# Kernel tuning notes

Hardware: AMD Instinct MI355X
Metric: run time of the kernel (lower is better)

Reference implementation:

```python
import jax, jax.numpy as jnp
import numpy as np

B, S, E, H, VP, L, T = 256, 256, 1024, 1024, 8, 64, 16


def setup_inputs() -> dict:
    key = jax.random.key(0)
    ks = jax.random.split(key, 10)
    image = jax.random.normal(ks[0], (B, S, E), jnp.float32)
    view_position = jax.random.uniform(ks[1], (B, VP), jnp.float32)
    label = (jax.random.uniform(ks[2], (B, T + 1, L)) > 0.5).astype(jnp.float32)
    # lengths sorted descending (length_sorted_rnn decorator), max forced to T+1
    length = jnp.sort(jax.random.randint(ks[3], (B,), 2, T + 2))[::-1]
    length = length.at[0].set(T + 1)
    def lin(k, out_d, in_d):
        return jax.random.normal(k, (out_d, in_d), jnp.float32) * (1.0 / np.sqrt(in_d)).astype(np.float32)
    IN = E + VP + 1 + L  # 1097: lstm_sizes = [embedding, view_position, 1, label]
    FC_OUT = L + H + 1 + 1  # 1090: fc_sizes = [label, hidden, 1, 1]
    return {
        'image': image, 'view_position': view_position, 'label': label, 'length': length,
        'W_h': lin(ks[4], H, E), 'b_h': jnp.zeros((H,), jnp.float32),
        'W_m': lin(ks[5], H, E), 'b_m': jnp.zeros((H,), jnp.float32),
        'W_ih': lin(ks[6], 4 * H, IN), 'W_hh': lin(ks[7], 4 * H, H),
        'b_ih': jnp.zeros((4 * H,), jnp.float32), 'b_hh': jnp.zeros((4 * H,), jnp.float32),
        'W_fc': lin(ks[8], FC_OUT, H), 'b_fc': jnp.zeros((FC_OUT,), jnp.float32),
    }


def reference(image, view_position, label, length, W_h, b_h, W_m, b_m,
              W_ih, W_hh, b_ih, b_hh, W_fc, b_fc):
    # Dropout is identity (inference). image: (B,S,E)
    image_mean = image.mean(axis=1)                      # (B,E)
    h0 = jnp.tanh(image_mean @ W_h.T + b_h)              # (B,H)
    m0 = jnp.tanh(image_mean @ W_m.T + b_m)              # (B,H)
    n_steps = label.shape[1] - 1
    bsz = image_mean.shape[0]

    def step(carry, inp):
        h, m = carry
        lab_t, t = inp
        begin = jnp.where(t == 0, 1.0, 0.0) * jnp.ones((bsz, 1), image_mean.dtype)
        x = jnp.concatenate([image_mean, view_position, begin, lab_t], axis=1)  # (B, 1097)
        gates = x @ W_ih.T + b_ih + h @ W_hh.T + b_hh    # (B, 4H)
        i, f, g, o = jnp.split(gates, 4, axis=1)
        m2 = jax.nn.sigmoid(f) * m + jax.nn.sigmoid(i) * jnp.tanh(g)
        h2 = jax.nn.sigmoid(o) * jnp.tanh(m2)
        out = h2 @ W_fc.T + b_fc                         # (B, L+H+2)
        topic = jax.nn.relu(out[:, L:L + H])
        stop = jax.nn.sigmoid(out[:, L + H:L + H + 1])
        temp = jnp.exp(out[:, L + H + 1:])
        return (h2, m2), jnp.concatenate([topic, stop, temp], axis=1)

    labels_tm = jnp.swapaxes(label[:, :n_steps], 0, 1)   # (T,B,L) time-major
    _, outs = jax.lax.scan(step, (h0, m0), (labels_tm, jnp.arange(n_steps)))
    # pad_sequence semantics: entries with t >= length-1 are zero padding
    mask = (jnp.arange(n_steps)[:, None] < (length - 1)[None, :]).astype(outs.dtype)
    return outs * mask[:, :, None]                       # (T, B, H+2) = [topic|stop|temp]
```

## Files before the change

### kernel.cpp

```cpp
#include <hip/hip_runtime.h>
#include <stdint.h>

typedef unsigned short u16;
typedef __attribute__((ext_vector_type(8))) short v8s;
typedef __attribute__((ext_vector_type(4))) float v4f;

__device__ __forceinline__ u16 f2bf(float f) {
  uint32_t x = __float_as_uint(f);
  return (u16)((x + 0x7fffu + ((x >> 16) & 1u)) >> 16);
}
__device__ __forceinline__ float bf2f(u16 u) {
  return __uint_as_float(((uint32_t)u) << 16);
}
__device__ __forceinline__ float sigf(float x) { return 1.f / (1.f + __expf(-x)); }

__device__ __forceinline__ v4f mfma16(v8s a, v8s b, v4f c) {
  return __builtin_amdgcn_mfma_f32_16x16x32_bf16(a, b, c, 0, 0, 0);
}

__device__ __forceinline__ void gll16(const u16* src, u16* ldsdst) {
  __builtin_amdgcn_global_load_lds(
      reinterpret_cast<__attribute__((address_space(1))) uint32_t*>(
          reinterpret_cast<uintptr_t>(src)),
      reinterpret_cast<__attribute__((address_space(3))) uint32_t*>(
          reinterpret_cast<uintptr_t>(ldsdst)),
      16, 0, 0);
}

__device__ __forceinline__ size_t fpoff(int row, int k, int KT) {
  return ((size_t)(((row >> 4) * KT + (k >> 6)) * 2 + ((k >> 5) & 1)) * 64 +
          ((k >> 3) & 3) * 16 + (row & 15)) * 8 + (k & 7);
}

__device__ __forceinline__ void load8(const float* p, float* f) {
  float4 a = *(const float4*)p;
  float4 b = *(const float4*)(p + 4);
  f[0]=a.x; f[1]=a.y; f[2]=a.z; f[3]=a.w; f[4]=b.x; f[5]=b.y; f[6]=b.z; f[7]=b.w;
}
__device__ __forceinline__ void store8bf(u16* dst, const float* f) {
  u16 t[8];
#pragma unroll
  for (int i = 0; i < 8; ++i) t[i] = f2bf(f[i]);
  *(v8s*)dst = *(const v8s*)t;
}

__global__ __launch_bounds__(256) void k_zero(unsigned* __restrict__ ctr) {
  ctr[blockIdx.x * 256 + threadIdx.x] = 0u;
}

__global__ __launch_bounds__(256) void k_convert_mean(
    const float* __restrict__ Wh, const float* __restrict__ Wm,
    const float* __restrict__ Wih, const float* __restrict__ Whh,
    const float* __restrict__ Wfc, const float* __restrict__ label,
    const float* __restrict__ image,
    u16* __restrict__ wcomb, u16* __restrict__ whhb, u16* __restrict__ wfcb,
    u16* __restrict__ wlabb, u16* __restrict__ labb,
    float4* __restrict__ pacc) {
  const int bid = blockIdx.x, tid = threadIdx.x;
  if (bid >= 5952) {
    int bi = bid - 5952;
    int b = bi >> 3, oct = bi & 7;
    const float4* src =
        (const float4*)image + (size_t)b * 65536 + (size_t)oct * 32 * 256 + tid;
    float4 s = make_float4(0.f, 0.f, 0.f, 0.f);
#pragma unroll 8
    for (int ss = 0; ss < 32; ++ss) {
      float4 v = src[(size_t)ss * 256];
      s.x += v.x; s.y += v.y; s.z += v.z; s.w += v.w;
    }
    pacc[(size_t)bi * 256 + tid] = s;
    return;
  }
  int64_t u = (int64_t)bid * 256 + tid;
  float f[8];
  if (u < 786432) {
    int lu = (int)u;
    int r15 = lu & 15, q = (lu >> 4) & 3, s = (lu >> 6) & 1, tile = lu >> 7;
    int tk = tile & 15, tr = tile >> 4;
    int row = tr * 16 + r15, k = tk * 64 + s * 32 + q * 8;
    if (row < 1024) load8(Wh + (size_t)row * 1024 + k, f);
    else if (row < 2048) load8(Wm + (size_t)(row - 1024) * 1024 + k, f);
    else {
      const float* p = Wih + (size_t)(row - 2048) * 1097 + k;
#pragma unroll
      for (int i = 0; i < 8; ++i) f[i] = p[i];
    }
    store8bf(wcomb + (size_t)lu * 8, f);
  } else if (u < 1310720) {
    int lu = (int)(u - 786432);
    int r15 = lu & 15, q = (lu >> 4) & 3, s = (lu >> 6) & 1, tile = lu >> 7;
    int tk = tile & 15, tr = tile >> 4;
    int row = tr * 16 + r15, k = tk * 64 + s * 32 + q * 8;
    load8(Whh + (size_t)row * 1024 + k, f);
    store8bf(whhb + (size_t)lu * 8, f);
  } else if (u < 1458176) {
    int lu = (int)(u - 1310720);
    int r15 = lu & 15, q = (lu >> 4) & 3, s = (lu >> 6) & 1, tile = lu >> 7;
    int tk = tile & 15, tr = tile >> 4;
    int row = tr * 16 + r15, k = tk * 64 + s * 32 + q * 8;
    if (row < 1090) load8(Wfc + (size_t)row * 1024 + k, f);
    else {
#pragma unroll
      for (int i = 0; i < 8; ++i) f[i] = 0.f;
    }
    store8bf(wfcb + (size_t)lu * 8, f);
  } else if (u < 1490944) {
    int lu = (int)(u - 1458176);
    int r15 = lu & 15, q = (lu >> 4) & 3, s = (lu >> 6) & 1, tile = lu >> 7;
    int row = tile * 16 + r15, k = s * 32 + q * 8;
    const float* p = Wih + (size_t)row * 1097 + 1033 + k;
#pragma unroll
    for (int i = 0; i < 8; ++i) f[i] = p[i];
    store8bf(wlabb + (size_t)lu * 8, f);
  } else {
    int lu = (int)(u - 1490944);
    int r15 = lu & 15, q = (lu >> 4) & 3, s = (lu >> 6) & 1, tile = lu >> 7;
    int row = tile * 16 + r15, k = s * 32 + q * 8;
    int t = row >> 8, b = row & 255;
    load8(label + ((size_t)b * 17 + t) * 64 + k, f);
    store8bf(labb + (size_t)lu * 8, f);
  }
}

__global__ __launch_bounds__(256) void k_mean2(const float4* __restrict__ pacc,
                                               u16* __restrict__ meanbf) {
  int b = blockIdx.x, tid = threadIdx.x;
  float4 s = make_float4(0.f, 0.f, 0.f, 0.f);
#pragma unroll
  for (int q = 0; q < 8; ++q) {
    float4 v = pacc[((size_t)b * 8 + q) * 256 + tid];
    s.x += v.x; s.y += v.y; s.z += v.z; s.w += v.w;
  }
  const float inv = 1.f / 256.f;
  int k = tid * 4;
  ushort4 o;
  o.x = f2bf(s.x * inv); o.y = f2bf(s.y * inv);
  o.z = f2bf(s.z * inv); o.w = f2bf(s.w * inv);
  *(ushort4*)&meanbf[fpoff(b, k, 16)] = o;
}

__global__ __launch_bounds__(256) void k_gemm_init(
    const u16* __restrict__ meanbf, const u16* __restrict__ wcomb,
    const float* __restrict__ bh, const float* __restrict__ bm,
    const float* __restrict__ bih, const float* __restrict__ bhh,
    const float* __restrict__ vp, const float* __restrict__ Wih,
    u16* __restrict__ hbuf, float* __restrict__ mbuf, float* __restrict__ basebuf) {
  __shared__ alignas(16) u16 lA[4 * 1024];
  __shared__ alignas(16) u16 lB[4 * 1024];
  const int tid = threadIdx.x, lane = tid & 63, wid = tid >> 6;
  const int bm0 = (blockIdx.x & 3) * 64;
  const int bn0 = (blockIdx.x >> 2) * 64;
  const int wr = wid >> 1, wc = wid & 1;
  v4f acc[2][2];
#pragma unroll
  for (int i = 0; i < 2; ++i)
#pragma unroll
    for (int j = 0; j < 2; ++j) acc[i][j] = (v4f){0.f, 0.f, 0.f, 0.f};

  for (int kt = 0; kt < 16; ++kt) {
    const u16* asrc = meanbf + ((size_t)((bm0 >> 4) + wid) * 16 + kt) * 1024 + lane * 8;
    gll16(asrc, lA + wid * 1024);
    gll16(asrc + 512, lA + wid * 1024 + 512);
    const u16* bsrc = wcomb + ((size_t)((bn0 >> 4) + wid) * 16 + kt) * 1024 + lane * 8;
    gll16(bsrc, lB + wid * 1024);
    gll16(bsrc + 512, lB + wid * 1024 + 512);
    __syncthreads();
#pragma unroll
    for (int s = 0; s < 2; ++s) {
      v8s a0 = *(const v8s*)&lA[(size_t)(wr * 2) * 1024 + s * 512 + lane * 8];
      v8s a1 = *(const v8s*)&lA[(size_t)(wr * 2 + 1) * 1024 + s * 512 + lane * 8];
      v8s b0 = *(const v8s*)&lB[(size_t)(wc * 2) * 1024 + s * 512 + lane * 8];
      v8s b1 = *(const v8s*)&lB[(size_t)(wc * 2 + 1) * 1024 + s * 512 + lane * 8];
      acc[0][0] = mfma16(a0, b0, acc[0][0]);
      acc[0][1] = mfma16(a0, b1, acc[0][1]);
      acc[1][0] = mfma16(a1, b0, acc[1][0]);
      acc[1][1] = mfma16(a1, b1, acc[1][1]);
    }
    __syncthreads();
  }
#pragma unroll
  for (int fm = 0; fm < 2; ++fm)
#pragma unroll
    for (int fn = 0; fn < 2; ++fn)
#pragma unroll
      for (int rg = 0; rg < 4; ++rg) {
        int row = bm0 + wr * 32 + fm * 16 + ((lane >> 4) << 2) + rg;
        int col = bn0 + wc * 32 + fn * 16 + (lane & 15);
        float v = acc[fm][fn][rg];
        if (col < 1024) {
          hbuf[fpoff(row, col, 16)] = f2bf(tanhf(v + bh[col]));
        } else if (col < 2048) {
          int nn = col - 1024;
          mbuf[(size_t)row * 1024 + nn] = tanhf(v + bm[nn]);
        } else {
          int j = col - 2048;
          float sv = v + bih[j] + bhh[j];
#pragma unroll
          for (int q = 0; q < 8; ++q)
            sv += vp[row * 8 + q] * Wih[(size_t)j * 1097 + 1024 + q];
          basebuf[(size_t)row * 4096 + j] = sv;
        }
      }
}

__global__ __launch_bounds__(256) void k_basefull(
    const u16* __restrict__ labb, const u16* __restrict__ wlabb,
    const float* __restrict__ basebuf, const float* __restrict__ Wih,
    u16* __restrict__ bfull) {
  __shared__ alignas(16) u16 lA[4 * 1024];
  __shared__ alignas(16) u16 lB[4 * 1024];
  const int tid = threadIdx.x, lane = tid & 63, wid = tid >> 6;
  const int bm0 = (blockIdx.x & 63) * 64;
  const int bn0 = (blockIdx.x >> 6) * 64;
  const int wr = wid >> 1, wc = wid & 1;
  v4f acc[2][2];
#pragma unroll
  for (int i = 0; i < 2; ++i)
#pragma unroll
    for (int j = 0; j < 2; ++j) acc[i][j] = (v4f){0.f, 0.f, 0.f, 0.f};

  const u16* asrc = labb + (size_t)((bm0 >> 4) + wid) * 1024 + lane * 8;
  gll16(asrc, lA + wid * 1024);
  gll16(asrc + 512, lA + wid * 1024 + 512);
  const u16* bsrc = wlabb + (size_t)((bn0 >> 4) + wid) * 1024 + lane * 8;
  gll16(bsrc, lB + wid * 1024);
  gll16(bsrc + 512, lB + wid * 1024 + 512);
  __syncthreads();
#pragma unroll
  for (int s = 0; s < 2; ++s) {
    v8s a0 = *(const v8s*)&lA[(size_t)(wr * 2) * 1024 + s * 512 + lane * 8];
    v8s a1 = *(const v8s*)&lA[(size_t)(wr * 2 + 1) * 1024 + s * 512 + lane * 8];
    v8s b0 = *(const v8s*)&lB[(size_t)(wc * 2) * 1024 + s * 512 + lane * 8];
    v8s b1 = *(const v8s*)&lB[(size_t)(wc * 2 + 1) * 1024 + s * 512 + lane * 8];
    acc[0][0] = mfma16(a0, b0, acc[0][0]);
    acc[0][1] = mfma16(a0, b1, acc[0][1]);
    acc[1][0] = mfma16(a1, b0, acc[1][0]);
    acc[1][1] = mfma16(a1, b1, acc[1][1]);
  }
#pragma unroll
  for (int fm = 0; fm < 2; ++fm)
#pragma unroll
    for (int fn = 0; fn < 2; ++fn)
#pragma unroll
      for (int rg = 0; rg < 4; ++rg) {
        int r = bm0 + wr * 32 + fm * 16 + ((lane >> 4) << 2) + rg;
        int j = bn0 + wc * 32 + fn * 16 + (lane & 15);
        int t = r >> 8, b = r & 255;
        float v = acc[fm][fn][rg] + basebuf[(size_t)b * 4096 + j];
        if (t == 0) v += Wih[(size_t)j * 1097 + 1032];
        bfull[(size_t)r * 4096 + j] = f2bf(v);
      }
}

__global__ __launch_bounds__(256, 1) void k_steps(
    const u16* __restrict__ whhb, const u16* __restrict__ bfull,
    const float* __restrict__ mbuf, u16* __restrict__ hbuf,
    unsigned* __restrict__ ctr) {
  __shared__ alignas(16) u16 lA[64 * 512];
  __shared__ alignas(16) float lact[4][32 * 33];
  const int tid = threadIdx.x, lane = tid & 63, wid = tid >> 6;
  const int blk = blockIdx.x;
  const int n0idx = (blk & 7) * 4 + (blk >> 6);
  const int n0 = n0idx * 32;
  const int grp = (blk >> 3) & 7;
  const int b0 = grp * 32;
  const int atr = b0 >> 4;

  const int tr0 = wid * 64 + (n0 >> 4);
  v8s breg[16][2][2];
#pragma unroll
  for (int kt = 0; kt < 16; ++kt)
#pragma unroll
    for (int s = 0; s < 2; ++s)
#pragma unroll
      for (int j = 0; j < 2; ++j)
        breg[kt][s][j] =
            *(const v8s*)&whhb[((size_t)(tr0 + j) * 16 + kt) * 1024 + s * 512 + lane * 8];

  const int rowm = tid >> 3;
  const int nql = (tid & 7) * 4;
  const int b = b0 + rowm;
  const int n = n0 + nql;
  float4 mreg = *(const float4*)&mbuf[(size_t)b * 1024 + n];

  for (int t = 0; t < 16; ++t) {
    if (t > 0) {
      const unsigned* f = &ctr[((t - 1) * 8 + grp) * 32];
      for (int it = 0; it < (1 << 18); ++it) {
        unsigned v = __hip_atomic_load(&f[lane & 31], __ATOMIC_RELAXED,
                                       __HIP_MEMORY_SCOPE_AGENT);
        if (__ballot(v == 0u) == 0ull) break;
        __builtin_amdgcn_s_sleep(1);
      }
    }
    const u16* hsrc = hbuf + (size_t)t * 262144;
#pragma unroll
    for (int ii = 0; ii < 16; ++ii) {
      const int c = wid * 16 + ii;
      const int i = c >> 5, kt = (c >> 1) & 15, s = c & 1;
      gll16(hsrc + ((size_t)(atr + i) * 16 + kt) * 1024 + s * 512 + lane * 8,
            lA + c * 512);
    }
    const u16* bb = bfull + (size_t)t * 1048576 + (size_t)b * 4096 + n;
    ushort4 ui = *(const ushort4*)(bb);
    ushort4 uf = *(const ushort4*)(bb + 1024);
    ushort4 ug = *(const ushort4*)(bb + 2048);
    ushort4 uo = *(const ushort4*)(bb + 3072);
    __syncthreads();

    v4f acc[2][2];
#pragma unroll
    for (int i = 0; i < 2; ++i)
#pragma unroll
      for (int j = 0; j < 2; ++j) acc[i][j] = (v4f){0.f, 0.f, 0.f, 0.f};
#pragma unroll
    for (int kt = 0; kt < 16; ++kt)
#pragma unroll
      for (int s = 0; s < 2; ++s) {
        v8s a0 = *(const v8s*)&lA[(size_t)((0 * 16 + kt) * 2 + s) * 512 + lane * 8];
        v8s a1 = *(const v8s*)&lA[(size_t)((1 * 16 + kt) * 2 + s) * 512 + lane * 8];
        acc[0][0] = mfma16(a0, breg[kt][s][0], acc[0][0]);
        acc[0][1] = mfma16(a0, breg[kt][s][1], acc[0][1]);
        acc[1][0] = mfma16(a1, breg[kt][s][0], acc[1][0]);
        acc[1][1] = mfma16(a1, breg[kt][s][1], acc[1][1]);
      }

#pragma unroll
    for (int fm = 0; fm < 2; ++fm)
#pragma unroll
      for (int fn = 0; fn < 2; ++fn)
#pragma unroll
        for (int rg = 0; rg < 4; ++rg) {
          int rr = fm * 16 + ((lane >> 4) << 2) + rg;
          int cc = fn * 16 + (lane & 15);
          lact[wid][rr * 33 + cc] = acc[fm][fn][rg];
        }
    __syncthreads();

    float m2a[4];
    u16 h2a[4];
#pragma unroll
    for (int q = 0; q < 4; ++q) {
      float gi = lact[0][rowm * 33 + nql + q] + bf2f(((const u16*)&ui)[q]);
      float gf = lact[1][rowm * 33 + nql + q] + bf2f(((const u16*)&uf)[q]);
      float gg = lact[2][rowm * 33 + nql + q] + bf2f(((const u16*)&ug)[q]);
      float go = lact[3][rowm * 33 + nql + q] + bf2f(((const u16*)&uo)[q]);
      float mov = ((const float*)&mreg)[q];
      float m2 = sigf(gf) * mov + sigf(gi) * tanhf(gg);
      float h2 = sigf(go) * tanhf(m2);
      m2a[q] = m2;
      h2a[q] = f2bf(h2);
    }
    mreg = make_float4(m2a[0], m2a[1], m2a[2], m2a[3]);
    ushort4 ho;
    ho.x = h2a[0]; ho.y = h2a[1]; ho.z = h2a[2]; ho.w = h2a[3];
    unsigned long long hv;
    __builtin_memcpy(&hv, &ho, 8);
    __hip_atomic_store(
        reinterpret_cast<unsigned long long*>(
            &hbuf[(size_t)(t + 1) * 262144 + fpoff(b, n, 16)]),
        hv, __ATOMIC_RELAXED, __HIP_MEMORY_SCOPE_AGENT);

    if (t < 15) {
      __syncthreads();
      if (tid == 0)
        __hip_atomic_store(&ctr[(t * 8 + grp) * 32 + n0idx], 1u,
                           __ATOMIC_RELAXED, __HIP_MEMORY_SCOPE_AGENT);
    }
  }
}

__global__ __launch_bounds__(256) void k_fc(
    const u16* __restrict__ hall, const u16* __restrict__ wfcb,
    const float* __restrict__ bfc, const int* __restrict__ length,
    float* __restrict__ out) {
  __shared__ alignas(16) u16 lA[4 * 1024];
  __shared__ alignas(16) u16 lB[4 * 1024];
  const int tid = threadIdx.x, lane = tid & 63, wid = tid >> 6;
  const int bm0 = (int)(blockIdx.x % 64) * 64;
  const int bn0 = (int)(blockIdx.x / 64) * 64;
  const int wr = wid >> 1, wc = wid & 1;
  v4f acc[2][2];
#pragma unroll
  for (int i = 0; i < 2; ++i)
#pragma unroll
    for (int j = 0; j < 2; ++j) acc[i][j] = (v4f){0.f, 0.f, 0.f, 0.f};

  for (int kt = 0; kt < 16; ++kt) {
    const u16* asrc = hall + ((size_t)((bm0 >> 4) + wid) * 16 + kt) * 1024 + lane * 8;
    gll16(asrc, lA + wid * 1024);
    gll16(asrc + 512, lA + wid * 1024 + 512);
    const u16* bsrc = wfcb + ((size_t)((bn0 >> 4) + wid) * 16 + kt) * 1024 + lane * 8;
    gll16(bsrc, lB + wid * 1024);
    gll16(bsrc + 512, lB + wid * 1024 + 512);
    __syncthreads();
#pragma unroll
    for (int s = 0; s < 2; ++s) {
      v8s a0 = *(const v8s*)&lA[(size_t)(wr * 2) * 1024 + s * 512 + lane * 8];
      v8s a1 = *(const v8s*)&lA[(size_t)(wr * 2 + 1) * 1024 + s * 512 + lane * 8];
      v8s b0 = *(const v8s*)&lB[(size_t)(wc * 2) * 1024 + s * 512 + lane * 8];
      v8s b1 = *(const v8s*)&lB[(size_t)(wc * 2 + 1) * 1024 + s * 512 + lane * 8];
      acc[0][0] = mfma16(a0, b0, acc[0][0]);
      acc[0][1] = mfma16(a0, b1, acc[0][1]);
      acc[1][0] = mfma16(a1, b0, acc[1][0]);
      acc[1][1] = mfma16(a1, b1, acc[1][1]);
    }
    __syncthreads();
  }
#pragma unroll
  for (int fm = 0; fm < 2; ++fm)
#pragma unroll
    for (int fn = 0; fn < 2; ++fn)
#pragma unroll
      for (int rg = 0; rg < 4; ++rg) {
        int r = bm0 + wr * 32 + fm * 16 + ((lane >> 4) << 2) + rg;
        int j = bn0 + wc * 32 + fn * 16 + (lane & 15);
        if (j < 64 || j >= 1090) continue;
        int t = r >> 8, b = r & 255;
        float v = acc[fm][fn][rg] + bfc[j];
        int c;
        if (j < 1088) { c = j - 64; v = fmaxf(v, 0.f); }
        else if (j == 1088) { c = 1024; v = 1.f / (1.f + expf(-v)); }
        else { c = 1025; v = expf(v); }
        if (t >= length[b] - 1) v = 0.f;
        out[((size_t)t * 256 + b) * 1026 + c] = v;
      }
}

extern "C" void kernel_launch(void* const* d_in, const int* in_sizes, int n_in,
                              void* d_out, int out_size, void* d_ws, size_t ws_size,
                              hipStream_t stream) {
  (void)in_sizes; (void)n_in; (void)out_size; (void)ws_size;
  const float* image  = (const float*)d_in[0];
  const float* vp     = (const float*)d_in[1];
  const float* label  = (const float*)d_in[2];
  const int*   length = (const int*)d_in[3];
  const float* Wh  = (const float*)d_in[4];
  const float* bh  = (const float*)d_in[5];
  const float* Wm  = (const float*)d_in[6];
  const float* bm  = (const float*)d_in[7];
  const float* Wih = (const float*)d_in[8];
  const float* Whh = (const float*)d_in[9];
  const float* bih = (const float*)d_in[10];
  const float* bhh = (const float*)d_in[11];
  const float* Wfc = (const float*)d_in[12];
  const float* bfc = (const float*)d_in[13];
  float* out = (float*)d_out;
  char* ws = (char*)d_ws;

  size_t off = 0;
  u16* wcomb  = (u16*)(ws + off); off += (size_t)6144 * 1024 * 2;
  u16* whhb   = (u16*)(ws + off); off += (size_t)4096 * 1024 * 2;
  u16* wfcb   = (u16*)(ws + off); off += (size_t)1152 * 1024 * 2;
  u16* wlabb  = (u16*)(ws + off); off += (size_t)4096 * 64 * 2;
  u16* labb   = (u16*)(ws + off); off += (size_t)4096 * 64 * 2;
  u16* meanbf = (u16*)(ws + off); off += (size_t)256 * 1024 * 2;
  u16* hbuf   = (u16*)(ws + off); off += (size_t)17 * 256 * 1024 * 2;
  float* mbuf    = (float*)(ws + off); off += (size_t)256 * 1024 * 4;
  float* basebuf = (float*)(ws + off); off += (size_t)256 * 4096 * 4;
  u16* bfull  = (u16*)(ws + off); off += (size_t)16 * 256 * 4096 * 2;
  unsigned* ctr = (unsigned*)(ws + off); off += 4096 * 4;
  float4* pacc = (float4*)bfull;

  k_zero<<<16, 256, 0, stream>>>(ctr);
  k_convert_mean<<<8000, 256, 0, stream>>>(Wh, Wm, Wih, Whh, Wfc, label, image,
                                           wcomb, whhb, wfcb, wlabb, labb, pacc);
  k_mean2<<<256, 256, 0, stream>>>(pacc, meanbf);
  k_gemm_init<<<384, 256, 0, stream>>>(meanbf, wcomb, bh, bm, bih, bhh, vp, Wih,
                                       hbuf, mbuf, basebuf);
  k_basefull<<<4096, 256, 0, stream>>>(labb, wlabb, basebuf, Wih, bfull);
  k_steps<<<256, 256, 0, stream>>>(whhb, bfull, mbuf, hbuf, ctr);
  k_fc<<<1152, 256, 0, stream>>>(hbuf + (size_t)256 * 1024, wfcb, bfc, length, out);
}
```

Baseline: 232.2 us.

## Split h-tile loads into two halves, stage gate bias via LDS, fold zeroing

The k_zero launch is removed and the counter zeroing is folded into extra blocks of k_convert_mean. In the recurrent step kernel, the LDS load of the hidden state is split into two K-halves with partial vmcnt waits, so MFMA work on the first half can start while the second half is still arriving. The per-step gate bias is now fetched by async global-to-LDS loads instead of per-thread register loads. The hand-written waitcnt counts and sched barriers are fragile and depend on the exact number of outstanding loads.

Result: faster. 225.6 us (-2.8%).

```diff
diff --git a/kernel.cpp b/kernel.cpp
--- a/kernel.cpp
+++ b/kernel.cpp
@@ -44,10 +44,6 @@
   *(v8s*)dst = *(const v8s*)t;
 }
 
-__global__ __launch_bounds__(256) void k_zero(unsigned* __restrict__ ctr) {
-  ctr[blockIdx.x * 256 + threadIdx.x] = 0u;
-}
-
 __global__ __launch_bounds__(256) void k_convert_mean(
     const float* __restrict__ Wh, const float* __restrict__ Wm,
     const float* __restrict__ Wih, const float* __restrict__ Whh,
@@ -55,8 +51,12 @@
     const float* __restrict__ image,
     u16* __restrict__ wcomb, u16* __restrict__ whhb, u16* __restrict__ wfcb,
     u16* __restrict__ wlabb, u16* __restrict__ labb,
-    float4* __restrict__ pacc) {
+    float4* __restrict__ pacc, unsigned* __restrict__ ctr) {
   const int bid = blockIdx.x, tid = threadIdx.x;
+  if (bid >= 8000) {
+    ctr[(bid - 8000) * 256 + tid] = 0u;
+    return;
+  }
   if (bid >= 5952) {
     int bi = bid - 5952;
     int b = bi >> 3, oct = bi & 7;
@@ -257,6 +257,7 @@
     const float* __restrict__ mbuf, u16* __restrict__ hbuf,
     unsigned* __restrict__ ctr) {
   __shared__ alignas(16) u16 lA[64 * 512];
+  __shared__ alignas(16) u16 lBias[8 * 512];
   __shared__ alignas(16) float lact[4][32 * 33];
   const int tid = threadIdx.x, lane = tid & 63, wid = tid >> 6;
   const int blk = blockIdx.x;
@@ -294,19 +295,35 @@
       }
     }
     const u16* hsrc = hbuf + (size_t)t * 262144;
-#pragma unroll
-    for (int ii = 0; ii < 16; ++ii) {
-      const int c = wid * 16 + ii;
-      const int i = c >> 5, kt = (c >> 1) & 15, s = c & 1;
+    __builtin_amdgcn_sched_barrier(0);
+#pragma unroll
+    for (int j = 0; j < 8; ++j) {
+      const int hc = wid * 8 + j;
+      const int i = hc >> 4, kt = (hc >> 1) & 7, s = hc & 1;
       gll16(hsrc + ((size_t)(atr + i) * 16 + kt) * 1024 + s * 512 + lane * 8,
-            lA + c * 512);
-    }
-    const u16* bb = bfull + (size_t)t * 1048576 + (size_t)b * 4096 + n;
-    ushort4 ui = *(const ushort4*)(bb);
-    ushort4 uf = *(const ushort4*)(bb + 1024);
-    ushort4 ug = *(const ushort4*)(bb + 2048);
-    ushort4 uo = *(const ushort4*)(bb + 3072);
-    __syncthreads();
+            lA + (i * 32 + kt * 2 + s) * 512);
+    }
+    __builtin_amdgcn_sched_barrier(0);
+#pragma unroll
+    for (int j = 0; j < 8; ++j) {
+      const int hc = wid * 8 + j;
+      const int i = hc >> 4, kt = ((hc >> 1) & 7) + 8, s = hc & 1;
+      gll16(hsrc + ((size_t)(atr + i) * 16 + kt) * 1024 + s * 512 + lane * 8,
+            lA + (i * 32 + kt * 2 + s) * 512);
+    }
+    __builtin_amdgcn_sched_barrier(0);
+#pragma unroll
+    for (int c2 = 0; c2 < 2; ++c2) {
+      const u16* bsrc = bfull + (size_t)t * 1048576 +
+                        (size_t)(b0 + c2 * 16 + (lane >> 2)) * 4096 +
+                        wid * 1024 + n0 + (lane & 3) * 8;
+      gll16(bsrc, lBias + (wid * 2 + c2) * 512);
+    }
+    __builtin_amdgcn_sched_barrier(0);
+    asm volatile("s_waitcnt vmcnt(10)" ::: "memory");
+    __builtin_amdgcn_sched_barrier(0);
+    __builtin_amdgcn_s_barrier();
+    __builtin_amdgcn_sched_barrier(0);
 
     v4f acc[2][2];
 #pragma unroll
@@ -314,7 +331,7 @@
 #pragma unroll
       for (int j = 0; j < 2; ++j) acc[i][j] = (v4f){0.f, 0.f, 0.f, 0.f};
 #pragma unroll
-    for (int kt = 0; kt < 16; ++kt)
+    for (int kt = 0; kt < 8; ++kt)
 #pragma unroll
       for (int s = 0; s < 2; ++s) {
         v8s a0 = *(const v8s*)&lA[(size_t)((0 * 16 + kt) * 2 + s) * 512 + lane * 8];
@@ -325,6 +342,23 @@
         acc[1][1] = mfma16(a1, breg[kt][s][1], acc[1][1]);
       }
 
+    __builtin_amdgcn_sched_barrier(0);
+    asm volatile("s_waitcnt vmcnt(2)" ::: "memory");
+    __builtin_amdgcn_sched_barrier(0);
+    __builtin_amdgcn_s_barrier();
+    __builtin_amdgcn_sched_barrier(0);
+#pragma unroll
+    for (int kt = 8; kt < 16; ++kt)
+#pragma unroll
+      for (int s = 0; s < 2; ++s) {
+        v8s a0 = *(const v8s*)&lA[(size_t)((0 * 16 + kt) * 2 + s) * 512 + lane * 8];
+        v8s a1 = *(const v8s*)&lA[(size_t)((1 * 16 + kt) * 2 + s) * 512 + lane * 8];
+        acc[0][0] = mfma16(a0, breg[kt][s][0], acc[0][0]);
+        acc[0][1] = mfma16(a0, breg[kt][s][1], acc[0][1]);
+        acc[1][0] = mfma16(a1, breg[kt][s][0], acc[1][0]);
+        acc[1][1] = mfma16(a1, breg[kt][s][1], acc[1][1]);
+      }
+
 #pragma unroll
     for (int fm = 0; fm < 2; ++fm)
 #pragma unroll
@@ -337,14 +371,16 @@
         }
     __syncthreads();
 
+    const int bofs = ((rowm & 15) * 4 + (nql >> 3)) * 8 + (nql & 7);
+    const int bch = (rowm >> 4) * 512;
     float m2a[4];
     u16 h2a[4];
 #pragma unroll
     for (int q = 0; q < 4; ++q) {
-      float gi = lact[0][rowm * 33 + nql + q] + bf2f(((const u16*)&ui)[q]);
-      float gf = lact[1][rowm * 33 + nql + q] + bf2f(((const u16*)&uf)[q]);
-      float gg = lact[2][rowm * 33 + nql + q] + bf2f(((const u16*)&ug)[q]);
-      float go = lact[3][rowm * 33 + nql + q] + bf2f(((const u16*)&uo)[q]);
+      float gi = lact[0][rowm * 33 + nql + q] + bf2f(lBias[0 * 1024 + bch + bofs + q]);
+      float gf = lact[1][rowm * 33 + nql + q] + bf2f(lBias[1 * 1024 + bch + bofs + q]);
+      float gg = lact[2][rowm * 33 + nql + q] + bf2f(lBias[2 * 1024 + bch + bofs + q]);
+      float go = lact[3][rowm * 33 + nql + q] + bf2f(lBias[3 * 1024 + bch + bofs + q]);
       float mov = ((const float*)&mreg)[q];
       float m2 = sigf(gf) * mov + sigf(gi) * tanhf(gg);
       float h2 = sigf(go) * tanhf(m2);
@@ -462,9 +498,8 @@
   unsigned* ctr = (unsigned*)(ws + off); off += 4096 * 4;
   float4* pacc = (float4*)bfull;
 
-  k_zero<<<16, 256, 0, stream>>>(ctr);
-  k_convert_mean<<<8000, 256, 0, stream>>>(Wh, Wm, Wih, Whh, Wfc, label, image,
-                                           wcomb, whhb, wfcb, wlabb, labb, pacc);
+  k_convert_mean<<<8016, 256, 0, stream>>>(Wh, Wm, Wih, Whh, Wfc, label, image,
+                                           wcomb, whhb, wfcb, wlabb, labb, pacc, ctr);
   k_mean2<<<256, 256, 0, stream>>>(pacc, meanbf);
   k_gemm_init<<<384, 256, 0, stream>>>(meanbf, wcomb, bh, bm, bih, bhh, vp, Wih,
                                        hbuf, mbuf, basebuf);
```
